# Performance work log

Measured on AMD Instinct MI355X. Metric: run time of the kernel, lower is better.

The kernel has to match this reference:

```python
import jax, jax.numpy as jnp
import numpy as np
from jax import lax

K = 3
LRELU_SLOPE = 0.2
GAIN = float(np.sqrt(2.0))


def setup_inputs() -> dict:
    key = jax.random.key(0)
    ks = jax.random.split(key, 7)
    B, Cin, Cout, H, W, S = 8, 64, 64, 256, 256, 512
    return {
        "x": jax.random.normal(ks[0], (B, Cin, H, W), dtype=jnp.float32),
        "style": jax.random.normal(ks[1], (B, S), dtype=jnp.float32),
        "noise": jax.random.normal(ks[2], (B, 1, H, W), dtype=jnp.float32),
        "weight": jax.random.normal(ks[3], (Cout, Cin, K, K), dtype=jnp.float32),
        "mod_w": jax.random.normal(ks[4], (S, Cin), dtype=jnp.float32),
        "mod_b": jnp.ones((Cin,), dtype=jnp.float32),
        "noise_weight": jax.random.uniform(ks[5], (1,), dtype=jnp.float32),
        "bias": jax.random.normal(ks[6], (Cout,), dtype=jnp.float32),
    }


def _styled_conv(x, style, noise, weight, mod_w, mod_b, noise_weight, bias):
    B, Cin, H, W = x.shape
    Cout = weight.shape[0]
    S = mod_w.shape[0]
    conv_scale = 1.0 / jnp.sqrt(jnp.float32(Cin * K * K))
    lin_scale = 1.0 / jnp.sqrt(jnp.float32(S))
    # EqualLinear modulation: [B, Cin]
    s = style @ (mod_w * lin_scale) + mod_b
    # per-sample modulated weights: [B, Cout, Cin, K, K]
    w = conv_scale * weight[None] * s[:, None, :, None, None]
    # demodulation over (Cin, K, K)
    demod = lax.rsqrt(jnp.sum(w * w, axis=(2, 3, 4)) + 1e-8)  # [B, Cout]
    w = w * demod[:, :, None, None, None]

    def conv_one(xi, wi):  # xi: [Cin,H,W], wi: [Cout,Cin,K,K]
        return lax.conv_general_dilated(
            xi[None], wi, window_strides=(1, 1),
            padding=[(K // 2, K // 2), (K // 2, K // 2)],
            dimension_numbers=("NCHW", "OIHW", "NCHW"))[0]

    out = jax.vmap(conv_one)(x, w)  # [B, Cout, H, W]
    out = out + noise_weight[0] * noise  # noise broadcast over channels
    out = jax.nn.leaky_relu(out + bias[None, :, None, None], LRELU_SLOPE) * GAIN
    return out


def reference(x, style, noise, weight, mod_w, mod_b, noise_weight, bias):
    return _styled_conv(x, style, noise, weight, mod_w, mod_b, noise_weight, bias)
```

## Files before the change

kernel.cpp:

```cpp
#include <hip/hip_runtime.h>
#include <hip/hip_bf16.h>

#define BB   8
#define CC   64
#define HH   256
#define WW   256
#define SS   512
#define HW   (HH*WW)

#define LIN_SCALE  0.044194173824159216f
#define CONV_SCALE 0.041666666666666664f
#define LRELU      0.2f
#define GAIN       1.4142135623730951f

#define TY 8
#define TX 32
#define LY (TY + 2)
#define LX (TX + 2)
#define WLE (9 * 8 * 64 * 8)

typedef __attribute__((ext_vector_type(8)))  short short8;
typedef __attribute__((ext_vector_type(16))) float floatx16;

static __device__ __forceinline__ unsigned short f2bf(float f) {
    unsigned u = __float_as_uint(f);
    u += 0x7FFF + ((u >> 16) & 1);
    return (unsigned short)(u >> 16);
}

static __device__ __forceinline__ unsigned pk2(float a, float b) {
    __hip_bfloat162 h = __float22bfloat162_rn(make_float2(a, b));
    return *(unsigned*)&h;
}

#define VC(vv,kk) ((kk)==0?(vv).x:((kk)==1?(vv).y:((kk)==2?(vv).z:(vv).w)))

__global__ void mod_kernel(const float* __restrict__ style,
                           const float* __restrict__ mod_w,
                           const float* __restrict__ mod_b,
                           float* __restrict__ s_out) {
    __shared__ float part[256];
    int b = blockIdx.x;
    int t = threadIdx.x;
    int ci = t & 63, kp = t >> 6;
    const float* st = style + b * SS + kp * 128;
    float acc = 0.f;
    for (int k = 0; k < 128; ++k)
        acc = fmaf(st[k], mod_w[(kp * 128 + k) * CC + ci], acc);
    part[t] = acc;
    __syncthreads();
    if (t < 64) {
        float v = part[t] + part[t + 64] + part[t + 128] + part[t + 192];
        s_out[b * CC + t] = v * LIN_SCALE + mod_b[t];
    }
}

__global__ void wmod_kernel(const float* __restrict__ weight,
                            const float* __restrict__ s_in,
                            unsigned short* __restrict__ wbf) {
    int bc = blockIdx.x;
    int b = bc >> 6, co = bc & 63;
    int ci = threadIdx.x;
    float wv[9];
    float sv = s_in[b * CC + ci] * CONV_SCALE;
    float sum = 0.f;
    const float* wp = weight + (co * CC + ci) * 9;
#pragma unroll
    for (int k = 0; k < 9; ++k) {
        wv[k] = wp[k] * sv;
        sum = fmaf(wv[k], wv[k], sum);
    }
#pragma unroll
    for (int off = 32; off; off >>= 1)
        sum += __shfl_xor(sum, off);
    float demod = rsqrtf(sum + 1e-8f);
    int g = ci >> 3, j = ci & 7;
#pragma unroll
    for (int ko = 0; ko < 9; ++ko) {
        size_t idx = ((((size_t)b * 9 + ko) * 8 + g) * 64 + co) * 8 + j;
        wbf[idx] = f2bf(wv[ko] * demod);
    }
}

__global__ __launch_bounds__(256, 3) void conv_kernel(
        const float* __restrict__ x,
        const float* __restrict__ noise,
        const float* __restrict__ nwp,
        const float* __restrict__ bias,
        const unsigned short* __restrict__ wbf,
        float* __restrict__ out) {
    __shared__ unsigned short xs[8 * LY * LX * 8];

    const int lin  = blockIdx.x;
    const int lin2 = (lin & 7) * 256 + (lin >> 3);
    const int b   = lin2 >> 8;
    const int rem = lin2 & 255;
    const int by  = rem >> 3;
    const int bx  = rem & 7;
    const int x0t = bx * TX;
    const int y0t = by * TY;

    const int t = threadIdx.x;
    const int lane = t & 63;
    const int wv = t >> 6;
    const int n31 = lane & 31;
    const int h   = lane >> 5;

    const unsigned short* wb = wbf + (size_t)b * WLE;
#define ALOAD(ko, kc, m) \
    (*(const short8*)&wb[((((ko) * 8 + (kc) * 2 + h) * 64) + (m) * 32 + n31) * 8])
    short8 a0c = ALOAD(0, 0, 0), a1c = ALOAD(0, 0, 1);
    short8 a0n = ALOAD(0, 1, 0), a1n = ALOAD(0, 1, 1);
    const float nw = nwp[0];
    float nzr0 = noise[(size_t)b * HW + (size_t)(y0t + wv * 2)     * WW + x0t + n31];
    float nzr1 = noise[(size_t)b * HW + (size_t)(y0t + wv * 2 + 1) * WW + x0t + n31];
    __builtin_amdgcn_sched_barrier(0);

#pragma unroll
    for (int bt = 0; bt < 2; ++bt) {
        int na = t + bt * 512;  na = na < 799 ? na : 799;
        int nb = na + 256;      nb = nb < 799 ? nb : 799;

        int qa = na % 10, ra = na / 10, yla = ra % 10, ga = ra / 10;
        int qb = nb % 10, rb = nb / 10, ylb = rb % 10, gb = rb / 10;
        int gya = y0t + yla - 1, gyb = y0t + ylb - 1;
        int gx0a = x0t - 4 + qa * 4, gx0b = x0t - 4 + qb * 4;
        bool rowoka = (unsigned)gya < (unsigned)HH;
        bool rowokb = (unsigned)gyb < (unsigned)HH;
        int gyca  = gya < 0 ? 0 : (gya > HH - 1 ? HH - 1 : gya);
        int gycb  = gyb < 0 ? 0 : (gyb > HH - 1 ? HH - 1 : gyb);
        int gx0ca = gx0a < 0 ? 0 : (gx0a > WW - 4 ? WW - 4 : gx0a);
        int gx0cb = gx0b < 0 ? 0 : (gx0b > WW - 4 ? WW - 4 : gx0b);
        const float* xpa = x + ((size_t)b * CC + ga * 8) * HW + (size_t)gyca * WW + gx0ca;
        const float* xpb = x + ((size_t)b * CC + gb * 8) * HW + (size_t)gycb * WW + gx0cb;

        float4 va[8], vb2[8];
#pragma unroll
        for (int j = 0; j < 8; ++j) va[j]  = *(const float4*)(xpa + (size_t)j * HW);
#pragma unroll
        for (int j = 0; j < 8; ++j) vb2[j] = *(const float4*)(xpb + (size_t)j * HW);
        __builtin_amdgcn_sched_barrier(0);

#pragma unroll
        for (int k = 0; k < 4; ++k) {
            int lx = 4 * qa - 3 + k;
            if ((unsigned)lx < (unsigned)LX) {
                bool ok = rowoka && ((unsigned)(gx0a + k) < (unsigned)WW);
                uint4 w;
                w.x = ok ? pk2(VC(va[0], k), VC(va[1], k)) : 0u;
                w.y = ok ? pk2(VC(va[2], k), VC(va[3], k)) : 0u;
                w.z = ok ? pk2(VC(va[4], k), VC(va[5], k)) : 0u;
                w.w = ok ? pk2(VC(va[6], k), VC(va[7], k)) : 0u;
                *(uint4*)&xs[((ga * LY + yla) * LX + lx) * 8] = w;
            }
        }
#pragma unroll
        for (int k = 0; k < 4; ++k) {
            int lx = 4 * qb - 3 + k;
            if ((unsigned)lx < (unsigned)LX) {
                bool ok = rowokb && ((unsigned)(gx0b + k) < (unsigned)WW);
                uint4 w;
                w.x = ok ? pk2(VC(vb2[0], k), VC(vb2[1], k)) : 0u;
                w.y = ok ? pk2(VC(vb2[2], k), VC(vb2[3], k)) : 0u;
                w.z = ok ? pk2(VC(vb2[4], k), VC(vb2[5], k)) : 0u;
                w.w = ok ? pk2(VC(vb2[6], k), VC(vb2[7], k)) : 0u;
                *(uint4*)&xs[((gb * LY + ylb) * LX + lx) * 8] = w;
            }
        }
    }
    __syncthreads();

    floatx16 acc[2][2];
    acc[0][0] = (floatx16)0.f; acc[0][1] = (floatx16)0.f;
    acc[1][0] = (floatx16)0.f; acc[1][1] = (floatx16)0.f;

#pragma unroll
    for (int ko = 0; ko < 9; ++ko) {
        const int kh = ko / 3, kw = ko % 3;
#pragma unroll
        for (int kc = 0; kc < 4; ++kc) {
            short8 p0 = a0n, p1 = a1n;
            {
                int s2 = ko * 4 + kc + 2;
                if (s2 <= 35) {
                    int pko = s2 >> 2, pkc = s2 & 3;
                    p0 = ALOAD(pko, pkc, 0);
                    p1 = ALOAD(pko, pkc, 1);
                }
            }
            const int g = kc * 2 + h;
#pragma unroll
            for (int rl = 0; rl < 2; ++rl) {
                int ys = wv * 2 + rl + kh;
                short8 bv = *(const short8*)&xs[((g * LY + ys) * LX + kw + n31) * 8];
                __builtin_amdgcn_s_setprio(1);
                acc[rl][0] = __builtin_amdgcn_mfma_f32_32x32x16_bf16(
                    a0c, bv, acc[rl][0], 0, 0, 0);
                acc[rl][1] = __builtin_amdgcn_mfma_f32_32x32x16_bf16(
                    a1c, bv, acc[rl][1], 0, 0, 0);
                __builtin_amdgcn_s_setprio(0);
            }
            a0c = a0n; a1c = a1n;
            a0n = p0;  a1n = p1;
        }
    }
#undef ALOAD

#pragma unroll
    for (int rl = 0; rl < 2; ++rl) {
        int py = y0t + wv * 2 + rl;
        float nz = nw * (rl ? nzr1 : nzr0);
#pragma unroll
        for (int reg = 0; reg < 16; ++reg) {
            int cr = (reg & 3) + 8 * (reg >> 2) + 4 * h;
            float v0 = acc[rl][0][reg] + nz + bias[cr];
            v0 = (v0 > 0.f ? v0 : LRELU * v0) * GAIN;
            out[((size_t)b * CC + cr) * HW + (size_t)py * WW + x0t + n31] = v0;
            float v1 = acc[rl][1][reg] + nz + bias[32 + cr];
            v1 = (v1 > 0.f ? v1 : LRELU * v1) * GAIN;
            out[((size_t)b * CC + 32 + cr) * HW + (size_t)py * WW + x0t + n31] = v1;
        }
    }
}

extern "C" void kernel_launch(void* const* d_in, const int* in_sizes, int n_in,
                              void* d_out, int out_size, void* d_ws, size_t ws_size,
                              hipStream_t stream) {
    const float* x       = (const float*)d_in[0];
    const float* style   = (const float*)d_in[1];
    const float* noise   = (const float*)d_in[2];
    const float* weight  = (const float*)d_in[3];
    const float* mod_w   = (const float*)d_in[4];
    const float* mod_b   = (const float*)d_in[5];
    const float* nw      = (const float*)d_in[6];
    const float* bias    = (const float*)d_in[7];
    float* out = (float*)d_out;

    float* s_buf          = (float*)d_ws;
    unsigned short* wbf   = (unsigned short*)((char*)d_ws + 4096);

    mod_kernel<<<dim3(BB), dim3(256), 0, stream>>>(style, mod_w, mod_b, s_buf);
    wmod_kernel<<<dim3(BB * CC), dim3(CC), 0, stream>>>(weight, s_buf, wbf);
    conv_kernel<<<dim3((WW / TX) * (HH / TY) * BB), dim3(256), 0, stream>>>(
        x, noise, nw, bias, wbf, out);
}
```

Baseline: 83.06 us.

## Split conv tile into two half-height stages with double-buffered LDS prefetch

Each block's 8-row tile is now processed as two 4-row halves. The global loads of x for the second half are issued before the MFMA loop of the first half runs, then converted and written into a second LDS buffer afterwards, so load latency overlaps compute. The epilogue store of the first half also overlaps this work. The trade-off is extra halo rows (6+6 instead of 10) and higher register pressure, and occupancy hints drop from 3 to 2 waves per SIMD. Weight fragments are reloaded for the second half.

```diff
diff --git a/kernel.cpp b/kernel.cpp
--- a/kernel.cpp
+++ b/kernel.cpp
@@ -14,9 +14,11 @@
 #define GAIN       1.4142135623730951f
 
 #define TY 8
+#define HY 4
 #define TX 32
-#define LY (TY + 2)
+#define LYH (HY + 2)
 #define LX (TX + 2)
+#define XSE (8 * LYH * LX * 8)
 #define WLE (9 * 8 * 64 * 8)
 
 typedef __attribute__((ext_vector_type(8)))  short short8;
@@ -82,14 +84,14 @@
     }
 }
 
-__global__ __launch_bounds__(256, 3) void conv_kernel(
+__global__ __launch_bounds__(256, 2) void conv_kernel(
         const float* __restrict__ x,
         const float* __restrict__ noise,
         const float* __restrict__ nwp,
         const float* __restrict__ bias,
         const unsigned short* __restrict__ wbf,
         float* __restrict__ out) {
-    __shared__ unsigned short xs[8 * LY * LX * 8];
+    __shared__ unsigned short xs[2][XSE];
 
     const int lin  = blockIdx.x;
     const int lin2 = (lin & 7) * 256 + (lin >> 3);
@@ -106,41 +108,39 @@
     const int n31 = lane & 31;
     const int h   = lane >> 5;
 
+    const int na = t < 479 ? t : 479;
+    const int nb = (t + 256) < 479 ? (t + 256) : 479;
+    const int qa = na % 10, ra = na / 10, yla = ra % 6, ga = ra / 6;
+    const int qb = nb % 10, rb = nb / 10, ylb = rb % 6, gb = rb / 6;
+    const int gx0a = x0t - 4 + qa * 4, gx0b = x0t - 4 + qb * 4;
+    const int gx0ca = gx0a < 0 ? 0 : (gx0a > WW - 4 ? WW - 4 : gx0a);
+    const int gx0cb = gx0b < 0 ? 0 : (gx0b > WW - 4 ? WW - 4 : gx0b);
+
     const unsigned short* wb = wbf + (size_t)b * WLE;
 #define ALOAD(ko, kc, m) \
     (*(const short8*)&wb[((((ko) * 8 + (kc) * 2 + h) * 64) + (m) * 32 + n31) * 8])
     short8 a0c = ALOAD(0, 0, 0), a1c = ALOAD(0, 0, 1);
     short8 a0n = ALOAD(0, 1, 0), a1n = ALOAD(0, 1, 1);
     const float nw = nwp[0];
-    float nzr0 = noise[(size_t)b * HW + (size_t)(y0t + wv * 2)     * WW + x0t + n31];
-    float nzr1 = noise[(size_t)b * HW + (size_t)(y0t + wv * 2 + 1) * WW + x0t + n31];
+    float nz0 = noise[(size_t)b * HW + (size_t)(y0t + wv)      * WW + x0t + n31];
+    float nz1 = noise[(size_t)b * HW + (size_t)(y0t + 4 + wv)  * WW + x0t + n31];
     __builtin_amdgcn_sched_barrier(0);
 
-#pragma unroll
-    for (int bt = 0; bt < 2; ++bt) {
-        int na = t + bt * 512;  na = na < 799 ? na : 799;
-        int nb = na + 256;      nb = nb < 799 ? nb : 799;
-
-        int qa = na % 10, ra = na / 10, yla = ra % 10, ga = ra / 10;
-        int qb = nb % 10, rb = nb / 10, ylb = rb % 10, gb = rb / 10;
-        int gya = y0t + yla - 1, gyb = y0t + ylb - 1;
-        int gx0a = x0t - 4 + qa * 4, gx0b = x0t - 4 + qb * 4;
+    {
+        const int y0h = y0t;
+        int gya = y0h + yla - 1, gyb = y0h + ylb - 1;
         bool rowoka = (unsigned)gya < (unsigned)HH;
         bool rowokb = (unsigned)gyb < (unsigned)HH;
-        int gyca  = gya < 0 ? 0 : (gya > HH - 1 ? HH - 1 : gya);
-        int gycb  = gyb < 0 ? 0 : (gyb > HH - 1 ? HH - 1 : gyb);
-        int gx0ca = gx0a < 0 ? 0 : (gx0a > WW - 4 ? WW - 4 : gx0a);
-        int gx0cb = gx0b < 0 ? 0 : (gx0b > WW - 4 ? WW - 4 : gx0b);
+        int gyca = gya < 0 ? 0 : (gya > HH - 1 ? HH - 1 : gya);
+        int gycb = gyb < 0 ? 0 : (gyb > HH - 1 ? HH - 1 : gyb);
         const float* xpa = x + ((size_t)b * CC + ga * 8) * HW + (size_t)gyca * WW + gx0ca;
         const float* xpb = x + ((size_t)b * CC + gb * 8) * HW + (size_t)gycb * WW + gx0cb;
-
         float4 va[8], vb2[8];
 #pragma unroll
         for (int j = 0; j < 8; ++j) va[j]  = *(const float4*)(xpa + (size_t)j * HW);
 #pragma unroll
         for (int j = 0; j < 8; ++j) vb2[j] = *(const float4*)(xpb + (size_t)j * HW);
         __builtin_amdgcn_sched_barrier(0);
-
 #pragma unroll
         for (int k = 0; k < 4; ++k) {
             int lx = 4 * qa - 3 + k;
@@ -151,7 +151,7 @@
                 w.y = ok ? pk2(VC(va[2], k), VC(va[3], k)) : 0u;
                 w.z = ok ? pk2(VC(va[4], k), VC(va[5], k)) : 0u;
                 w.w = ok ? pk2(VC(va[6], k), VC(va[7], k)) : 0u;
-                *(uint4*)&xs[((ga * LY + yla) * LX + lx) * 8] = w;
+                *(uint4*)&xs[0][((ga * LYH + yla) * LX + lx) * 8] = w;
             }
         }
 #pragma unroll
@@ -164,63 +164,146 @@
                 w.y = ok ? pk2(VC(vb2[2], k), VC(vb2[3], k)) : 0u;
                 w.z = ok ? pk2(VC(vb2[4], k), VC(vb2[5], k)) : 0u;
                 w.w = ok ? pk2(VC(vb2[6], k), VC(vb2[7], k)) : 0u;
-                *(uint4*)&xs[((gb * LY + ylb) * LX + lx) * 8] = w;
+                *(uint4*)&xs[0][((gb * LYH + ylb) * LX + lx) * 8] = w;
             }
         }
     }
     __syncthreads();
 
-    floatx16 acc[2][2];
-    acc[0][0] = (floatx16)0.f; acc[0][1] = (floatx16)0.f;
-    acc[1][0] = (floatx16)0.f; acc[1][1] = (floatx16)0.f;
-
-#pragma unroll
-    for (int ko = 0; ko < 9; ++ko) {
-        const int kh = ko / 3, kw = ko % 3;
-#pragma unroll
-        for (int kc = 0; kc < 4; ++kc) {
-            short8 p0 = a0n, p1 = a1n;
-            {
-                int s2 = ko * 4 + kc + 2;
-                if (s2 <= 35) {
-                    int pko = s2 >> 2, pkc = s2 & 3;
-                    p0 = ALOAD(pko, pkc, 0);
-                    p1 = ALOAD(pko, pkc, 1);
+    const int y1h = y0t + HY;
+    int gya1 = y1h + yla - 1, gyb1 = y1h + ylb - 1;
+    bool rowoka1 = (unsigned)gya1 < (unsigned)HH;
+    bool rowokb1 = (unsigned)gyb1 < (unsigned)HH;
+    int gyca1 = gya1 < 0 ? 0 : (gya1 > HH - 1 ? HH - 1 : gya1);
+    int gycb1 = gyb1 < 0 ? 0 : (gyb1 > HH - 1 ? HH - 1 : gyb1);
+    {
+        const float* xpa = x + ((size_t)b * CC + ga * 8) * HW + (size_t)gyca1 * WW + gx0ca;
+        const float* xpb = x + ((size_t)b * CC + gb * 8) * HW + (size_t)gycb1 * WW + gx0cb;
+        float4 wa[8], wb2[8];
+#pragma unroll
+        for (int j = 0; j < 8; ++j) wa[j]  = *(const float4*)(xpa + (size_t)j * HW);
+#pragma unroll
+        for (int j = 0; j < 8; ++j) wb2[j] = *(const float4*)(xpb + (size_t)j * HW);
+        __builtin_amdgcn_sched_barrier(0);
+
+        floatx16 acc[2];
+        acc[0] = (floatx16)0.f; acc[1] = (floatx16)0.f;
+#pragma unroll
+        for (int ko = 0; ko < 9; ++ko) {
+            const int kh = ko / 3, kw = ko % 3;
+#pragma unroll
+            for (int kc = 0; kc < 4; ++kc) {
+                short8 p0 = a0n, p1 = a1n;
+                {
+                    int s2 = ko * 4 + kc + 2;
+                    if (s2 <= 35) {
+                        int pko = s2 >> 2, pkc = s2 & 3;
+                        p0 = ALOAD(pko, pkc, 0);
+                        p1 = ALOAD(pko, pkc, 1);
+                    }
                 }
-            }
-            const int g = kc * 2 + h;
-#pragma unroll
-            for (int rl = 0; rl < 2; ++rl) {
-                int ys = wv * 2 + rl + kh;
-                short8 bv = *(const short8*)&xs[((g * LY + ys) * LX + kw + n31) * 8];
+                const int g = kc * 2 + h;
+                int ys = wv + kh;
+                short8 bv = *(const short8*)&xs[0][((g * LYH + ys) * LX + kw + n31) * 8];
                 __builtin_amdgcn_s_setprio(1);
-                acc[rl][0] = __builtin_amdgcn_mfma_f32_32x32x16_bf16(
-                    a0c, bv, acc[rl][0], 0, 0, 0);
-                acc[rl][1] = __builtin_amdgcn_mfma_f32_32x32x16_bf16(
-                    a1c, bv, acc[rl][1], 0, 0, 0);
+                acc[0] = __builtin_amdgcn_mfma_f32_32x32x16_bf16(a0c, bv, acc[0], 0, 0, 0);
+                acc[1] = __builtin_amdgcn_mfma_f32_32x32x16_bf16(a1c, bv, acc[1], 0, 0, 0);
                 __builtin_amdgcn_s_setprio(0);
-            }
-            a0c = a0n; a1c = a1n;
-            a0n = p0;  a1n = p1;
-        }
-    }
-#undef ALOAD
-
-#pragma unroll
-    for (int rl = 0; rl < 2; ++rl) {
-        int py = y0t + wv * 2 + rl;
-        float nz = nw * (rl ? nzr1 : nzr0);
+                a0c = a0n; a1c = a1n;
+                a0n = p0;  a1n = p1;
+            }
+        }
+        __builtin_amdgcn_sched_barrier(0);
+
+#pragma unroll
+        for (int k = 0; k < 4; ++k) {
+            int lx = 4 * qa - 3 + k;
+            if ((unsigned)lx < (unsigned)LX) {
+                bool ok = rowoka1 && ((unsigned)(gx0a + k) < (unsigned)WW);
+                uint4 w;
+                w.x = ok ? pk2(VC(wa[0], k), VC(wa[1], k)) : 0u;
+                w.y = ok ? pk2(VC(wa[2], k), VC(wa[3], k)) : 0u;
+                w.z = ok ? pk2(VC(wa[4], k), VC(wa[5], k)) : 0u;
+                w.w = ok ? pk2(VC(wa[6], k), VC(wa[7], k)) : 0u;
+                *(uint4*)&xs[1][((ga * LYH + yla) * LX + lx) * 8] = w;
+            }
+        }
+#pragma unroll
+        for (int k = 0; k < 4; ++k) {
+            int lx = 4 * qb - 3 + k;
+            if ((unsigned)lx < (unsigned)LX) {
+                bool ok = rowokb1 && ((unsigned)(gx0b + k) < (unsigned)WW);
+                uint4 w;
+                w.x = ok ? pk2(VC(wb2[0], k), VC(wb2[1], k)) : 0u;
+                w.y = ok ? pk2(VC(wb2[2], k), VC(wb2[3], k)) : 0u;
+                w.z = ok ? pk2(VC(wb2[4], k), VC(wb2[5], k)) : 0u;
+                w.w = ok ? pk2(VC(wb2[6], k), VC(wb2[7], k)) : 0u;
+                *(uint4*)&xs[1][((gb * LYH + ylb) * LX + lx) * 8] = w;
+            }
+        }
+
+        {
+            int py = y0t + wv;
+            float nz = nw * nz0;
+#pragma unroll
+            for (int reg = 0; reg < 16; ++reg) {
+                int cr = (reg & 3) + 8 * (reg >> 2) + 4 * h;
+                float v0 = acc[0][reg] + nz + bias[cr];
+                v0 = (v0 > 0.f ? v0 : LRELU * v0) * GAIN;
+                out[((size_t)b * CC + cr) * HW + (size_t)py * WW + x0t + n31] = v0;
+                float v1 = acc[1][reg] + nz + bias[32 + cr];
+                v1 = (v1 > 0.f ? v1 : LRELU * v1) * GAIN;
+                out[((size_t)b * CC + 32 + cr) * HW + (size_t)py * WW + x0t + n31] = v1;
+            }
+        }
+    }
+    __syncthreads();
+
+    {
+        short8 b0c = ALOAD(0, 0, 0), b1c = ALOAD(0, 0, 1);
+        short8 b0n = ALOAD(0, 1, 0), b1n = ALOAD(0, 1, 1);
+        floatx16 acc[2];
+        acc[0] = (floatx16)0.f; acc[1] = (floatx16)0.f;
+#pragma unroll
+        for (int ko = 0; ko < 9; ++ko) {
+            const int kh = ko / 3, kw = ko % 3;
+#pragma unroll
+            for (int kc = 0; kc < 4; ++kc) {
+                short8 p0 = b0n, p1 = b1n;
+                {
+                    int s2 = ko * 4 + kc + 2;
+                    if (s2 <= 35) {
+                        int pko = s2 >> 2, pkc = s2 & 3;
+                        p0 = ALOAD(pko, pkc, 0);
+                        p1 = ALOAD(pko, pkc, 1);
+                    }
+                }
+                const int g = kc * 2 + h;
+                int ys = wv + kh;
+                short8 bv = *(const short8*)&xs[1][((g * LYH + ys) * LX + kw + n31) * 8];
+                __builtin_amdgcn_s_setprio(1);
+                acc[0] = __builtin_amdgcn_mfma_f32_32x32x16_bf16(b0c, bv, acc[0], 0, 0, 0);
+                acc[1] = __builtin_amdgcn_mfma_f32_32x32x16_bf16(b1c, bv, acc[1], 0, 0, 0);
+                __builtin_amdgcn_s_setprio(0);
+                b0c = b0n; b1c = b1n;
+                b0n = p0;  b1n = p1;
+            }
+        }
+
+        int py = y1h + wv;
+        float nz = nw * nz1;
 #pragma unroll
         for (int reg = 0; reg < 16; ++reg) {
             int cr = (reg & 3) + 8 * (reg >> 2) + 4 * h;
-            float v0 = acc[rl][0][reg] + nz + bias[cr];
+            float v0 = acc[0][reg] + nz + bias[cr];
             v0 = (v0 > 0.f ? v0 : LRELU * v0) * GAIN;
             out[((size_t)b * CC + cr) * HW + (size_t)py * WW + x0t + n31] = v0;
-            float v1 = acc[rl][1][reg] + nz + bias[32 + cr];
+            float v1 = acc[1][reg] + nz + bias[32 + cr];
             v1 = (v1 > 0.f ? v1 : LRELU * v1) * GAIN;
             out[((size_t)b * CC + 32 + cr) * HW + (size_t)py * WW + x0t + n31] = v1;
         }
     }
+#undef ALOAD
 }
 
 extern "C" void kernel_launch(void* const* d_in, const int* in_sizes, int n_in,
```

After: 169.1 us. 2.04x slower.
